# Performance work log

Measured on AMD Instinct MI355X. Metric: run time of the kernel, lower is better.

Reference implementation:

```python
import jax, jax.numpy as jnp
import numpy as np

N_NODES = 50000
N_EDGES = 800000
D_IN = 96
D_HID = 96
D_OUT = 4


def _glorot(key, shape):
    lim = float(np.sqrt(6.0 / (shape[0] + shape[1])))
    return jax.random.uniform(key, shape, jnp.float32, -lim, lim)


def setup_inputs() -> dict:
    key = jax.random.key(0)
    ks = jax.random.split(key, 8)
    x = jax.random.normal(ks[0], (N_NODES, D_IN), jnp.float32)
    edge_index = jax.random.randint(ks[1], (2, N_EDGES), 0, N_NODES, jnp.int64)
    return {
        'x': x,
        'edge_index': edge_index,
        'W0': _glorot(ks[2], (D_IN, D_HID)), 'b0': jnp.zeros((D_HID,), jnp.float32),
        'W1': _glorot(ks[3], (D_HID, D_HID)), 'b1': jnp.zeros((D_HID,), jnp.float32),
        'W2': _glorot(ks[4], (D_HID, D_HID)), 'b2': jnp.zeros((D_HID,), jnp.float32),
        'Wfc': _glorot(ks[5], (D_HID, D_OUT)), 'bfc': jnp.zeros((D_OUT,), jnp.float32),
    }


def _gcn_conv(x, src, dst, W, b, n):
    # GCNConv: linear transform, add self-loops, symmetric degree norm, scatter-add.
    h = x @ W                                   # [N, D]
    loops = jnp.arange(n, dtype=src.dtype)
    s = jnp.concatenate([src, loops])           # [E+N]
    d = jnp.concatenate([dst, loops])
    deg = jax.ops.segment_sum(jnp.ones_like(d, dtype=h.dtype), d, num_segments=n)
    dinv = jnp.where(deg > 0, jax.lax.rsqrt(deg), 0.0)
    norm = dinv[s] * dinv[d]                    # [E+N]
    msgs = h[s] * norm[:, None]                 # gather + scale
    out = jax.ops.segment_sum(msgs, d, num_segments=n)  # scatter-add
    return out + b


def reference(x, edge_index, W0, b0, W1, b1, W2, b2, Wfc, bfc):
    src, dst = edge_index[0], edge_index[1]
    n = x.shape[0]
    h = jax.nn.relu(_gcn_conv(x, src, dst, W0, b0, n))   # dropout = identity (eval)
    h = jax.nn.relu(_gcn_conv(h, src, dst, W1, b1, n))
    h = jax.nn.relu(_gcn_conv(h, src, dst, W2, b2, n))
    return h @ Wfc + bfc
```

## Files before the change

### kernel.cpp

```cpp
#include <hip/hip_runtime.h>

typedef __bf16 bf16x8 __attribute__((ext_vector_type(8)));
typedef float  f32x4  __attribute__((ext_vector_type(4)));
typedef float  f32x8  __attribute__((ext_vector_type(8)));
typedef unsigned short ushort;
typedef ushort us8 __attribute__((ext_vector_type(8)));

constexpr int N_NODES = 50000;
constexpr int N_EDGES = 800000;
constexpr int SLOTS = 64;
constexpr int GE   = N_EDGES / 256;
constexpr int WBLK = (3 * 9216) / 256;
constexpr int GMF  = (N_NODES + 63) / 64;

__device__ inline float h16f(ushort u) {
    union { _Float16 h; ushort u; } cv; cv.u = u; return (float)cv.h;
}
__device__ inline ushort f16b(float f) {
    union { _Float16 h; ushort u; } cv; cv.h = (_Float16)f; return cv.u;
}
__device__ inline ushort bf16b(float f) {
    union { __bf16 b; ushort u; } cv; cv.b = (__bf16)f; return cv.u;
}
__device__ inline f32x8 bf8_to_f32(us8 u) {
    f32x8 r;
#pragma unroll
    for (int i = 0; i < 8; ++i) r[i] = __uint_as_float(((unsigned int)u[i]) << 16);
    return r;
}

__global__ __launch_bounds__(256) void k_count(const int* __restrict__ dst,
                                               int* __restrict__ cnt,
                                               ushort* __restrict__ rank,
                                               const float* __restrict__ W0,
                                               const float* __restrict__ W1,
                                               const float* __restrict__ W2,
                                               ushort* __restrict__ Wt) {
    const int b = blockIdx.x;
    if (b < GE) {
        int e = b * 256 + threadIdx.x;
        rank[e] = (ushort)atomicAdd(&cnt[dst[e]], 1);
    } else {
        int i = (b - GE) * 256 + threadIdx.x;
        int m = i / 9216, li = i - m * 9216;
        const float* W = (m == 0) ? W0 : (m == 1) ? W1 : W2;
        int k = li / 96, c = li - k * 96;
        Wt[m * 9216 + c * 96 + k] = bf16b(W[li]);
    }
}

__device__ __forceinline__ void mfma_store(const ushort* sX, const ushort* sW,
                                           ushort* __restrict__ Y, int rowbase) {
    const int tid = threadIdx.x;
    const int wv = tid >> 6, lane = tid & 63, quad = lane >> 4, l16 = lane & 15;
    f32x4 acc[6];
#pragma unroll
    for (int t = 0; t < 6; ++t) acc[t] = (f32x4){0.f, 0.f, 0.f, 0.f};

    const ushort* ax = sX + (wv * 16 + l16) * 96 + quad * 8;
#pragma unroll
    for (int s = 0; s < 3; ++s) {
        bf16x8 a = *(const bf16x8*)(ax + s * 32);
#pragma unroll
        for (int t = 0; t < 6; ++t) {
            bf16x8 b = *(const bf16x8*)(sW + (t * 16 + l16) * 96 + s * 32 + quad * 8);
            acc[t] = __builtin_amdgcn_mfma_f32_16x16x32_bf16(a, b, acc[t], 0, 0, 0);
        }
    }
    const int r0 = rowbase + wv * 16 + quad * 4;
#pragma unroll
    for (int t = 0; t < 6; ++t) {
#pragma unroll
        for (int g = 0; g < 4; ++g) {
            int r = r0 + g;
            if (r < N_NODES) Y[(size_t)r * 96 + t * 16 + l16] = bf16b(acc[t][g]);
        }
    }
}

__global__ __launch_bounds__(256) void k_fill_gemm1(const int* __restrict__ src,
                                                    const int* __restrict__ dst,
                                                    const int* __restrict__ cnt,
                                                    const ushort* __restrict__ rank,
                                                    unsigned int* __restrict__ csr,
                                                    const float* __restrict__ x,
                                                    const ushort* __restrict__ Wt,
                                                    ushort* __restrict__ H) {
    __shared__ ushort sS[64 * 96 + 96 * 96];
    const int b = blockIdx.x;
    const int tid = threadIdx.x;
    if (b < GE) {
        int e = b * 256 + tid;
        int s = src[e], d = dst[e];
        float hs = rsqrtf((float)(cnt[s] + 1));
        unsigned int entry = (unsigned int)(ushort)s | ((unsigned int)f16b(hs) << 16);
        csr[(size_t)d * SLOTS + rank[e]] = entry;
    } else {
        ushort* sX = sS;
        ushort* sW = sS + 64 * 96;
        const int rowbase = (b - GE) * 64;
        for (int i = tid; i < 9216 / 8; i += 256)
            ((uint4*)sW)[i] = ((const uint4*)Wt)[i];
        for (int i = tid; i < 64 * 24; i += 256) {
            int r = i / 24, c4 = i % 24;
            int gr = rowbase + r;
            float4 v = make_float4(0.f, 0.f, 0.f, 0.f);
            if (gr < N_NODES) v = ((const float4*)(x + (size_t)gr * 96))[c4];
            ushort* p = sX + r * 96 + c4 * 4;
            p[0] = bf16b(v.x); p[1] = bf16b(v.y); p[2] = bf16b(v.z); p[3] = bf16b(v.w);
        }
        __syncthreads();
        mfma_store(sX, sW, H, rowbase);
    }
}

__global__ __launch_bounds__(768) void k_agg_gemm(const ushort* __restrict__ A,
                                                  const int* __restrict__ cnt,
                                                  const unsigned int* __restrict__ csr,
                                                  const float* __restrict__ bias,
                                                  const ushort* __restrict__ Wt,
                                                  ushort* __restrict__ Y) {
    __shared__ ushort sS[64 * 96 + 96 * 96];
    ushort* sX = sS;
    ushort* sW = sS + 64 * 96;
    const int tid = threadIdx.x;
    const int rowbase = blockIdx.x * 64;

    for (int i = tid; i < 9216 / 8; i += 768)
        ((uint4*)sW)[i] = ((const uint4*)Wt)[i];

    const int g = tid / 12;
    const int c = tid - g * 12;
    const int n = rowbase + g;

    f32x8 acc = (f32x8){0.f, 0.f, 0.f, 0.f, 0.f, 0.f, 0.f, 0.f};
    if (n < N_NODES) {
        const int deg = cnt[n];
        const float dn = rsqrtf((float)(deg + 1));
        us8 a0 = *(const us8*)(A + (size_t)n * 96 + c * 8);
        acc = bf8_to_f32(a0) * (dn * dn);

        const unsigned int* row = csr + (size_t)n * SLOTS;
        int j = 0;
        for (; j + 8 <= deg; j += 8) {
            const uint4 q0 = *(const uint4*)(row + j);
            const uint4 q1 = *(const uint4*)(row + j + 4);
            const us8 u0 = *(const us8*)(A + (size_t)(q0.x & 0xFFFFu) * 96 + c * 8);
            const us8 u1 = *(const us8*)(A + (size_t)(q0.y & 0xFFFFu) * 96 + c * 8);
            const us8 u2 = *(const us8*)(A + (size_t)(q0.z & 0xFFFFu) * 96 + c * 8);
            const us8 u3 = *(const us8*)(A + (size_t)(q0.w & 0xFFFFu) * 96 + c * 8);
            const us8 u4 = *(const us8*)(A + (size_t)(q1.x & 0xFFFFu) * 96 + c * 8);
            const us8 u5 = *(const us8*)(A + (size_t)(q1.y & 0xFFFFu) * 96 + c * 8);
            const us8 u6 = *(const us8*)(A + (size_t)(q1.z & 0xFFFFu) * 96 + c * 8);
            const us8 u7 = *(const us8*)(A + (size_t)(q1.w & 0xFFFFu) * 96 + c * 8);
            acc += bf8_to_f32(u0) * (h16f((ushort)(q0.x >> 16)) * dn);
            acc += bf8_to_f32(u1) * (h16f((ushort)(q0.y >> 16)) * dn);
            acc += bf8_to_f32(u2) * (h16f((ushort)(q0.z >> 16)) * dn);
            acc += bf8_to_f32(u3) * (h16f((ushort)(q0.w >> 16)) * dn);
            acc += bf8_to_f32(u4) * (h16f((ushort)(q1.x >> 16)) * dn);
            acc += bf8_to_f32(u5) * (h16f((ushort)(q1.y >> 16)) * dn);
            acc += bf8_to_f32(u6) * (h16f((ushort)(q1.z >> 16)) * dn);
            acc += bf8_to_f32(u7) * (h16f((ushort)(q1.w >> 16)) * dn);
        }
        for (; j + 4 <= deg; j += 4) {
            const uint4 q = *(const uint4*)(row + j);
            const us8 u0 = *(const us8*)(A + (size_t)(q.x & 0xFFFFu) * 96 + c * 8);
            const us8 u1 = *(const us8*)(A + (size_t)(q.y & 0xFFFFu) * 96 + c * 8);
            const us8 u2 = *(const us8*)(A + (size_t)(q.z & 0xFFFFu) * 96 + c * 8);
            const us8 u3 = *(const us8*)(A + (size_t)(q.w & 0xFFFFu) * 96 + c * 8);
            acc += bf8_to_f32(u0) * (h16f((ushort)(q.x >> 16)) * dn);
            acc += bf8_to_f32(u1) * (h16f((ushort)(q.y >> 16)) * dn);
            acc += bf8_to_f32(u2) * (h16f((ushort)(q.z >> 16)) * dn);
            acc += bf8_to_f32(u3) * (h16f((ushort)(q.w >> 16)) * dn);
        }
        for (; j < deg; ++j) {
            const unsigned int e = row[j];
            const float w = h16f((ushort)(e >> 16)) * dn;
            const us8 u = *(const us8*)(A + (size_t)(e & 0xFFFFu) * 96 + c * 8);
            acc += bf8_to_f32(u) * w;
        }
#pragma unroll
        for (int f = 0; f < 8; ++f) acc[f] = fmaxf(acc[f] + bias[c * 8 + f], 0.0f);
    }
    {
        us8 o;
#pragma unroll
        for (int f = 0; f < 8; ++f) o[f] = bf16b(acc[f]);
        *(us8*)(sX + g * 96 + c * 8) = o;
    }
    __syncthreads();

    const int wv = tid >> 6;
    const int lane = tid & 63, quad = lane >> 4, l16 = lane & 15;
    const int t0 = 2 * wv;
    const int rg = t0 / 6;
    const int ct0 = t0 - rg * 6;

    f32x4 acc0 = (f32x4){0.f, 0.f, 0.f, 0.f};
    f32x4 acc1 = (f32x4){0.f, 0.f, 0.f, 0.f};
    const ushort* ax = sX + (rg * 16 + l16) * 96 + quad * 8;
#pragma unroll
    for (int s = 0; s < 3; ++s) {
        bf16x8 a = *(const bf16x8*)(ax + s * 32);
        bf16x8 b0 = *(const bf16x8*)(sW + (ct0 * 16 + l16) * 96 + s * 32 + quad * 8);
        bf16x8 b1 = *(const bf16x8*)(sW + ((ct0 + 1) * 16 + l16) * 96 + s * 32 + quad * 8);
        acc0 = __builtin_amdgcn_mfma_f32_16x16x32_bf16(a, b0, acc0, 0, 0, 0);
        acc1 = __builtin_amdgcn_mfma_f32_16x16x32_bf16(a, b1, acc1, 0, 0, 0);
    }
    const int r0 = rowbase + rg * 16 + quad * 4;
#pragma unroll
    for (int gg = 0; gg < 4; ++gg) {
        int r = r0 + gg;
        if (r < N_NODES) {
            Y[(size_t)r * 96 + ct0 * 16 + l16]       = bf16b(acc0[gg]);
            Y[(size_t)r * 96 + (ct0 + 1) * 16 + l16] = bf16b(acc1[gg]);
        }
    }
}

template<int MODE>
__global__ __launch_bounds__(192) void k_agg(const ushort* __restrict__ A,
                                             const int* __restrict__ cnt,
                                             const unsigned int* __restrict__ csr,
                                             const float* __restrict__ bias,
                                             ushort* __restrict__ Hout,
                                             float* __restrict__ out4,
                                             const float* __restrict__ Wfc,
                                             const float* __restrict__ bfc) {
    __shared__ float sWfc[384];
    __shared__ float red[16][12][4];
    const int tid = threadIdx.x;
    if (MODE == 1) {
        for (int i = tid; i < 384; i += 192) sWfc[i] = Wfc[i];
        __syncthreads();
    }
    const int g = tid / 12, c = tid % 12;
    const int n = blockIdx.x * 16 + g;

    const int deg = cnt[n];
    const float dn = rsqrtf((float)(deg + 1));
    us8 a0 = *(const us8*)(A + (size_t)n * 96 + c * 8);
    f32x8 acc = bf8_to_f32(a0) * (dn * dn);

    const unsigned int* row = csr + (size_t)n * SLOTS;
    int j = 0;
    for (; j + 8 <= deg; j += 8) {
        const uint4 q0 = *(const uint4*)(row + j);
        const uint4 q1 = *(const uint4*)(row + j + 4);
        const us8 u0 = *(const us8*)(A + (size_t)(q0.x & 0xFFFFu) * 96 + c * 8);
        const us8 u1 = *(const us8*)(A + (size_t)(q0.y & 0xFFFFu) * 96 + c * 8);
        const us8 u2 = *(const us8*)(A + (size_t)(q0.z & 0xFFFFu) * 96 + c * 8);
        const us8 u3 = *(const us8*)(A + (size_t)(q0.w & 0xFFFFu) * 96 + c * 8);
        const us8 u4 = *(const us8*)(A + (size_t)(q1.x & 0xFFFFu) * 96 + c * 8);
        const us8 u5 = *(const us8*)(A + (size_t)(q1.y & 0xFFFFu) * 96 + c * 8);
        const us8 u6 = *(const us8*)(A + (size_t)(q1.z & 0xFFFFu) * 96 + c * 8);
        const us8 u7 = *(const us8*)(A + (size_t)(q1.w & 0xFFFFu) * 96 + c * 8);
        acc += bf8_to_f32(u0) * (h16f((ushort)(q0.x >> 16)) * dn);
        acc += bf8_to_f32(u1) * (h16f((ushort)(q0.y >> 16)) * dn);
        acc += bf8_to_f32(u2) * (h16f((ushort)(q0.z >> 16)) * dn);
        acc += bf8_to_f32(u3) * (h16f((ushort)(q0.w >> 16)) * dn);
        acc += bf8_to_f32(u4) * (h16f((ushort)(q1.x >> 16)) * dn);
        acc += bf8_to_f32(u5) * (h16f((ushort)(q1.y >> 16)) * dn);
        acc += bf8_to_f32(u6) * (h16f((ushort)(q1.z >> 16)) * dn);
        acc += bf8_to_f32(u7) * (h16f((ushort)(q1.w >> 16)) * dn);
    }
    for (; j + 4 <= deg; j += 4) {
        const uint4 q = *(const uint4*)(row + j);
        const us8 u0 = *(const us8*)(A + (size_t)(q.x & 0xFFFFu) * 96 + c * 8);
        const us8 u1 = *(const us8*)(A + (size_t)(q.y & 0xFFFFu) * 96 + c * 8);
        const us8 u2 = *(const us8*)(A + (size_t)(q.z & 0xFFFFu) * 96 + c * 8);
        const us8 u3 = *(const us8*)(A + (size_t)(q.w & 0xFFFFu) * 96 + c * 8);
        acc += bf8_to_f32(u0) * (h16f((ushort)(q.x >> 16)) * dn);
        acc += bf8_to_f32(u1) * (h16f((ushort)(q.y >> 16)) * dn);
        acc += bf8_to_f32(u2) * (h16f((ushort)(q.z >> 16)) * dn);
        acc += bf8_to_f32(u3) * (h16f((ushort)(q.w >> 16)) * dn);
    }
    for (; j < deg; ++j) {
        const unsigned int e = row[j];
        const float w = h16f((ushort)(e >> 16)) * dn;
        const us8 u = *(const us8*)(A + (size_t)(e & 0xFFFFu) * 96 + c * 8);
        acc += bf8_to_f32(u) * w;
    }
#pragma unroll
    for (int f = 0; f < 8; ++f) acc[f] = fmaxf(acc[f] + bias[c * 8 + f], 0.0f);

    if (MODE == 0) {
        us8 o;
#pragma unroll
        for (int f = 0; f < 8; ++f) o[f] = bf16b(acc[f]);
        *(us8*)(Hout + (size_t)n * 96 + c * 8) = o;
    } else {
        float p0 = 0.f, p1 = 0.f, p2 = 0.f, p3 = 0.f;
#pragma unroll
        for (int f = 0; f < 8; ++f) {
            const float* wr = sWfc + (c * 8 + f) * 4;
            p0 += acc[f] * wr[0];
            p1 += acc[f] * wr[1];
            p2 += acc[f] * wr[2];
            p3 += acc[f] * wr[3];
        }
        red[g][c][0] = p0; red[g][c][1] = p1; red[g][c][2] = p2; red[g][c][3] = p3;
        __syncthreads();
        if (tid < 64) {
            const int gg = tid >> 2, jj = tid & 3;
            float s = bfc[jj];
#pragma unroll
            for (int cc = 0; cc < 12; ++cc) s += red[gg][cc][jj];
            out4[(size_t)(blockIdx.x * 16 + gg) * 4 + jj] = s;
        }
    }
}

extern "C" void kernel_launch(void* const* d_in, const int* in_sizes, int n_in,
                              void* d_out, int out_size, void* d_ws, size_t ws_size,
                              hipStream_t stream) {
    const float* x   = (const float*)d_in[0];
    const int*   ei  = (const int*)d_in[1];
    const int*   src = ei;
    const int*   dst = ei + N_EDGES;
    const float* W0  = (const float*)d_in[2];
    const float* b0  = (const float*)d_in[3];
    const float* W1  = (const float*)d_in[4];
    const float* b1  = (const float*)d_in[5];
    const float* W2  = (const float*)d_in[6];
    const float* b2  = (const float*)d_in[7];
    const float* Wfc = (const float*)d_in[8];
    const float* bfc = (const float*)d_in[9];
    float* out = (float*)d_out;

    char* w = (char*)d_ws;
    unsigned int* csr = (unsigned int*)w;  w += ((size_t)N_NODES * SLOTS * 4 + 15) & ~15ULL;
    int*    cnt  = (int*)w;                w += ((size_t)N_NODES * 4 + 15) & ~15ULL;
    ushort* rank = (ushort*)w;             w += ((size_t)N_EDGES * 2 + 15) & ~15ULL;
    ushort* Wt   = (ushort*)w;             w += ((size_t)3 * 9216 * 2 + 15) & ~15ULL;
    ushort* H    = (ushort*)w;             w += ((size_t)N_NODES * 96 * 2 + 15) & ~15ULL;
    ushort* G    = (ushort*)w;

    const int gAgg = N_NODES / 16;

    (void)hipMemsetAsync(cnt, 0, (size_t)N_NODES * 4, stream);
    hipLaunchKernelGGL(k_count, dim3(GE + WBLK), dim3(256), 0, stream,
                       dst, cnt, rank, W0, W1, W2, Wt);
    hipLaunchKernelGGL(k_fill_gemm1, dim3(GE + GMF), dim3(256), 0, stream,
                       src, dst, cnt, rank, csr, x, Wt, H);
    hipLaunchKernelGGL(k_agg_gemm, dim3(GMF), dim3(768), 0, stream,
                       H, cnt, csr, b0, Wt + 9216, G);
    hipLaunchKernelGGL(k_agg_gemm, dim3(GMF), dim3(768), 0, stream,
                       G, cnt, csr, b1, Wt + 2 * 9216, H);
    hipLaunchKernelGGL((k_agg<1>), dim3(gAgg), dim3(192), 0, stream,
                       H, cnt, csr, b2, (ushort*)nullptr, out, Wfc, bfc);
}
```

Before: 224.5 us.

## Merge degree count and CSR fill into one pass, store 16-bit neighbor ids

Merges the count and fill kernels into one. Each edge atomically claims its slot and writes only a 16-bit source id, so the separate rank array and the precomputed fp16 per-edge norm go away. The aggregation kernels now look up the source degree from cnt for each neighbor instead of reading a packed norm, and they process 32 nodes per block with 384 threads. W0 is transposed inside each GEMM block, while W1 and W2 are converted by extra blocks. This drops one launch and halves CSR bytes, at the cost of an extra scattered cnt read per edge and redundant W0 conversion in every GEMM block.

```diff
diff --git a/kernel.cpp b/kernel.cpp
--- a/kernel.cpp
+++ b/kernel.cpp
@@ -5,20 +5,17 @@
 typedef float  f32x8  __attribute__((ext_vector_type(8)));
 typedef unsigned short ushort;
 typedef ushort us8 __attribute__((ext_vector_type(8)));
+typedef ushort us4 __attribute__((ext_vector_type(4)));
 
 constexpr int N_NODES = 50000;
 constexpr int N_EDGES = 800000;
 constexpr int SLOTS = 64;
 constexpr int GE   = N_EDGES / 256;
-constexpr int WBLK = (3 * 9216) / 256;
 constexpr int GMF  = (N_NODES + 63) / 64;
-
-__device__ inline float h16f(ushort u) {
-    union { _Float16 h; ushort u; } cv; cv.u = u; return (float)cv.h;
-}
-__device__ inline ushort f16b(float f) {
-    union { _Float16 h; ushort u; } cv; cv.h = (_Float16)f; return cv.u;
-}
+constexpr int WBLK = (2 * 9216) / 256;
+constexpr int AGG_NODES = 32;
+constexpr int GAGG = (N_NODES + AGG_NODES - 1) / AGG_NODES;
+
 __device__ inline ushort bf16b(float f) {
     union { __bf16 b; ushort u; } cv; cv.b = (__bf16)f; return cv.u;
 }
@@ -28,25 +25,8 @@
     for (int i = 0; i < 8; ++i) r[i] = __uint_as_float(((unsigned int)u[i]) << 16);
     return r;
 }
-
-__global__ __launch_bounds__(256) void k_count(const int* __restrict__ dst,
-                                               int* __restrict__ cnt,
-                                               ushort* __restrict__ rank,
-                                               const float* __restrict__ W0,
-                                               const float* __restrict__ W1,
-                                               const float* __restrict__ W2,
-                                               ushort* __restrict__ Wt) {
-    const int b = blockIdx.x;
-    if (b < GE) {
-        int e = b * 256 + threadIdx.x;
-        rank[e] = (ushort)atomicAdd(&cnt[dst[e]], 1);
-    } else {
-        int i = (b - GE) * 256 + threadIdx.x;
-        int m = i / 9216, li = i - m * 9216;
-        const float* W = (m == 0) ? W0 : (m == 1) ? W1 : W2;
-        int k = li / 96, c = li - k * 96;
-        Wt[m * 9216 + c * 96 + k] = bf16b(W[li]);
-    }
+__device__ inline float invdeg(const int* cnt, int s) {
+    return rsqrtf((float)(cnt[s] + 1));
 }
 
 __device__ __forceinline__ void mfma_store(const ushort* sX, const ushort* sW,
@@ -78,29 +58,32 @@
     }
 }
 
-__global__ __launch_bounds__(256) void k_fill_gemm1(const int* __restrict__ src,
-                                                    const int* __restrict__ dst,
-                                                    const int* __restrict__ cnt,
-                                                    const ushort* __restrict__ rank,
-                                                    unsigned int* __restrict__ csr,
-                                                    const float* __restrict__ x,
-                                                    const ushort* __restrict__ Wt,
-                                                    ushort* __restrict__ H) {
+__global__ __launch_bounds__(256) void k_count_gemm1(const int* __restrict__ src,
+                                                     const int* __restrict__ dst,
+                                                     int* __restrict__ cnt,
+                                                     ushort* __restrict__ csr,
+                                                     const float* __restrict__ x,
+                                                     const float* __restrict__ W0,
+                                                     const float* __restrict__ W1,
+                                                     const float* __restrict__ W2,
+                                                     ushort* __restrict__ Wt,
+                                                     ushort* __restrict__ H) {
     __shared__ ushort sS[64 * 96 + 96 * 96];
     const int b = blockIdx.x;
     const int tid = threadIdx.x;
     if (b < GE) {
         int e = b * 256 + tid;
-        int s = src[e], d = dst[e];
-        float hs = rsqrtf((float)(cnt[s] + 1));
-        unsigned int entry = (unsigned int)(ushort)s | ((unsigned int)f16b(hs) << 16);
-        csr[(size_t)d * SLOTS + rank[e]] = entry;
-    } else {
+        int d = dst[e];
+        int r = atomicAdd(&cnt[d], 1);
+        csr[(size_t)d * SLOTS + r] = (ushort)src[e];
+    } else if (b < GE + GMF) {
         ushort* sX = sS;
         ushort* sW = sS + 64 * 96;
         const int rowbase = (b - GE) * 64;
-        for (int i = tid; i < 9216 / 8; i += 256)
-            ((uint4*)sW)[i] = ((const uint4*)Wt)[i];
+        for (int i = tid; i < 9216; i += 256) {
+            int k = i / 96, cc = i - k * 96;
+            sW[cc * 96 + k] = bf16b(W0[i]);
+        }
         for (int i = tid; i < 64 * 24; i += 256) {
             int r = i / 24, c4 = i % 24;
             int gr = rowbase + r;
@@ -111,22 +94,28 @@
         }
         __syncthreads();
         mfma_store(sX, sW, H, rowbase);
-    }
-}
-
-__global__ __launch_bounds__(768) void k_agg_gemm(const ushort* __restrict__ A,
-                                                  const int* __restrict__ cnt,
-                                                  const unsigned int* __restrict__ csr,
-                                                  const float* __restrict__ bias,
-                                                  const ushort* __restrict__ Wt,
-                                                  ushort* __restrict__ Y) {
-    __shared__ ushort sS[64 * 96 + 96 * 96];
+    } else {
+        int i = (b - GE - GMF) * 256 + tid;
+        int m = i / 9216, li = i - m * 9216;
+        const float* W = (m == 0) ? W1 : W2;
+        int k = li / 96, cc = li - k * 96;
+        Wt[(m + 1) * 9216 + cc * 96 + k] = bf16b(W[li]);
+    }
+}
+
+__global__ __launch_bounds__(384, 4) void k_agg_gemm(const ushort* __restrict__ A,
+                                                     const int* __restrict__ cnt,
+                                                     const ushort* __restrict__ csr,
+                                                     const float* __restrict__ bias,
+                                                     const ushort* __restrict__ Wt,
+                                                     ushort* __restrict__ Y) {
+    __shared__ ushort sS[AGG_NODES * 96 + 96 * 96];
     ushort* sX = sS;
-    ushort* sW = sS + 64 * 96;
+    ushort* sW = sS + AGG_NODES * 96;
     const int tid = threadIdx.x;
-    const int rowbase = blockIdx.x * 64;
-
-    for (int i = tid; i < 9216 / 8; i += 768)
+    const int rowbase = blockIdx.x * AGG_NODES;
+
+    for (int i = tid; i < 9216 / 8; i += 384)
         ((uint4*)sW)[i] = ((const uint4*)Wt)[i];
 
     const int g = tid / 12;
@@ -138,47 +127,49 @@
         const int deg = cnt[n];
         const float dn = rsqrtf((float)(deg + 1));
         us8 a0 = *(const us8*)(A + (size_t)n * 96 + c * 8);
-        acc = bf8_to_f32(a0) * (dn * dn);
-
-        const unsigned int* row = csr + (size_t)n * SLOTS;
+
+        f32x8 nb = (f32x8){0.f, 0.f, 0.f, 0.f, 0.f, 0.f, 0.f, 0.f};
+        const ushort* row = csr + (size_t)n * SLOTS;
         int j = 0;
         for (; j + 8 <= deg; j += 8) {
-            const uint4 q0 = *(const uint4*)(row + j);
-            const uint4 q1 = *(const uint4*)(row + j + 4);
-            const us8 u0 = *(const us8*)(A + (size_t)(q0.x & 0xFFFFu) * 96 + c * 8);
-            const us8 u1 = *(const us8*)(A + (size_t)(q0.y & 0xFFFFu) * 96 + c * 8);
-            const us8 u2 = *(const us8*)(A + (size_t)(q0.z & 0xFFFFu) * 96 + c * 8);
-            const us8 u3 = *(const us8*)(A + (size_t)(q0.w & 0xFFFFu) * 96 + c * 8);
-            const us8 u4 = *(const us8*)(A + (size_t)(q1.x & 0xFFFFu) * 96 + c * 8);
-            const us8 u5 = *(const us8*)(A + (size_t)(q1.y & 0xFFFFu) * 96 + c * 8);
-            const us8 u6 = *(const us8*)(A + (size_t)(q1.z & 0xFFFFu) * 96 + c * 8);
-            const us8 u7 = *(const us8*)(A + (size_t)(q1.w & 0xFFFFu) * 96 + c * 8);
-            acc += bf8_to_f32(u0) * (h16f((ushort)(q0.x >> 16)) * dn);
-            acc += bf8_to_f32(u1) * (h16f((ushort)(q0.y >> 16)) * dn);
-            acc += bf8_to_f32(u2) * (h16f((ushort)(q0.z >> 16)) * dn);
-            acc += bf8_to_f32(u3) * (h16f((ushort)(q0.w >> 16)) * dn);
-            acc += bf8_to_f32(u4) * (h16f((ushort)(q1.x >> 16)) * dn);
-            acc += bf8_to_f32(u5) * (h16f((ushort)(q1.y >> 16)) * dn);
-            acc += bf8_to_f32(u6) * (h16f((ushort)(q1.z >> 16)) * dn);
-            acc += bf8_to_f32(u7) * (h16f((ushort)(q1.w >> 16)) * dn);
+            const us8 q = *(const us8*)(row + j);
+            const int s0 = q[0], s1 = q[1], s2 = q[2], s3 = q[3];
+            const int s4 = q[4], s5 = q[5], s6 = q[6], s7 = q[7];
+            const us8 u0 = *(const us8*)(A + (size_t)s0 * 96 + c * 8);
+            const us8 u1 = *(const us8*)(A + (size_t)s1 * 96 + c * 8);
+            const us8 u2 = *(const us8*)(A + (size_t)s2 * 96 + c * 8);
+            const us8 u3 = *(const us8*)(A + (size_t)s3 * 96 + c * 8);
+            const us8 u4 = *(const us8*)(A + (size_t)s4 * 96 + c * 8);
+            const us8 u5 = *(const us8*)(A + (size_t)s5 * 96 + c * 8);
+            const us8 u6 = *(const us8*)(A + (size_t)s6 * 96 + c * 8);
+            const us8 u7 = *(const us8*)(A + (size_t)s7 * 96 + c * 8);
+            nb += bf8_to_f32(u0) * invdeg(cnt, s0);
+            nb += bf8_to_f32(u1) * invdeg(cnt, s1);
+            nb += bf8_to_f32(u2) * invdeg(cnt, s2);
+            nb += bf8_to_f32(u3) * invdeg(cnt, s3);
+            nb += bf8_to_f32(u4) * invdeg(cnt, s4);
+            nb += bf8_to_f32(u5) * invdeg(cnt, s5);
+            nb += bf8_to_f32(u6) * invdeg(cnt, s6);
+            nb += bf8_to_f32(u7) * invdeg(cnt, s7);
         }
         for (; j + 4 <= deg; j += 4) {
-            const uint4 q = *(const uint4*)(row + j);
-            const us8 u0 = *(const us8*)(A + (size_t)(q.x & 0xFFFFu) * 96 + c * 8);
-            const us8 u1 = *(const us8*)(A + (size_t)(q.y & 0xFFFFu) * 96 + c * 8);
-            const us8 u2 = *(const us8*)(A + (size_t)(q.z & 0xFFFFu) * 96 + c * 8);
-            const us8 u3 = *(const us8*)(A + (size_t)(q.w & 0xFFFFu) * 96 + c * 8);
-            acc += bf8_to_f32(u0) * (h16f((ushort)(q.x >> 16)) * dn);
-            acc += bf8_to_f32(u1) * (h16f((ushort)(q.y >> 16)) * dn);
-            acc += bf8_to_f32(u2) * (h16f((ushort)(q.z >> 16)) * dn);
-            acc += bf8_to_f32(u3) * (h16f((ushort)(q.w >> 16)) * dn);
+            const us4 q = *(const us4*)(row + j);
+            const int s0 = q[0], s1 = q[1], s2 = q[2], s3 = q[3];
+            const us8 u0 = *(const us8*)(A + (size_t)s0 * 96 + c * 8);
+            const us8 u1 = *(const us8*)(A + (size_t)s1 * 96 + c * 8);
+            const us8 u2 = *(const us8*)(A + (size_t)s2 * 96 + c * 8);
+            const us8 u3 = *(const us8*)(A + (size_t)s3 * 96 + c * 8);
+            nb += bf8_to_f32(u0) * invdeg(cnt, s0);
+            nb += bf8_to_f32(u1) * invdeg(cnt, s1);
+            nb += bf8_to_f32(u2) * invdeg(cnt, s2);
+            nb += bf8_to_f32(u3) * invdeg(cnt, s3);
         }
         for (; j < deg; ++j) {
-            const unsigned int e = row[j];
-            const float w = h16f((ushort)(e >> 16)) * dn;
-            const us8 u = *(const us8*)(A + (size_t)(e & 0xFFFFu) * 96 + c * 8);
-            acc += bf8_to_f32(u) * w;
-        }
+            const int s = row[j];
+            const us8 u = *(const us8*)(A + (size_t)s * 96 + c * 8);
+            nb += bf8_to_f32(u) * invdeg(cnt, s);
+        }
+        acc = (nb + bf8_to_f32(a0) * dn) * dn;
 #pragma unroll
         for (int f = 0; f < 8; ++f) acc[f] = fmaxf(acc[f] + bias[c * 8 + f], 0.0f);
     }
@@ -218,96 +209,87 @@
     }
 }
 
-template<int MODE>
-__global__ __launch_bounds__(192) void k_agg(const ushort* __restrict__ A,
-                                             const int* __restrict__ cnt,
-                                             const unsigned int* __restrict__ csr,
-                                             const float* __restrict__ bias,
-                                             ushort* __restrict__ Hout,
-                                             float* __restrict__ out4,
-                                             const float* __restrict__ Wfc,
-                                             const float* __restrict__ bfc) {
+__global__ __launch_bounds__(192) void k_agg_fc(const ushort* __restrict__ A,
+                                                const int* __restrict__ cnt,
+                                                const ushort* __restrict__ csr,
+                                                const float* __restrict__ bias,
+                                                float* __restrict__ out4,
+                                                const float* __restrict__ Wfc,
+                                                const float* __restrict__ bfc) {
     __shared__ float sWfc[384];
     __shared__ float red[16][12][4];
     const int tid = threadIdx.x;
-    if (MODE == 1) {
-        for (int i = tid; i < 384; i += 192) sWfc[i] = Wfc[i];
-        __syncthreads();
-    }
+    for (int i = tid; i < 384; i += 192) sWfc[i] = Wfc[i];
+    __syncthreads();
     const int g = tid / 12, c = tid % 12;
     const int n = blockIdx.x * 16 + g;
 
     const int deg = cnt[n];
     const float dn = rsqrtf((float)(deg + 1));
     us8 a0 = *(const us8*)(A + (size_t)n * 96 + c * 8);
-    f32x8 acc = bf8_to_f32(a0) * (dn * dn);
-
-    const unsigned int* row = csr + (size_t)n * SLOTS;
+
+    f32x8 nb = (f32x8){0.f, 0.f, 0.f, 0.f, 0.f, 0.f, 0.f, 0.f};
+    const ushort* row = csr + (size_t)n * SLOTS;
     int j = 0;
     for (; j + 8 <= deg; j += 8) {
-        const uint4 q0 = *(const uint4*)(row + j);
-        const uint4 q1 = *(const uint4*)(row + j + 4);
-        const us8 u0 = *(const us8*)(A + (size_t)(q0.x & 0xFFFFu) * 96 + c * 8);
-        const us8 u1 = *(const us8*)(A + (size_t)(q0.y & 0xFFFFu) * 96 + c * 8);
-        const us8 u2 = *(const us8*)(A + (size_t)(q0.z & 0xFFFFu) * 96 + c * 8);
-        const us8 u3 = *(const us8*)(A + (size_t)(q0.w & 0xFFFFu) * 96 + c * 8);
-        const us8 u4 = *(const us8*)(A + (size_t)(q1.x & 0xFFFFu) * 96 + c * 8);
-        const us8 u5 = *(const us8*)(A + (size_t)(q1.y & 0xFFFFu) * 96 + c * 8);
-        const us8 u6 = *(const us8*)(A + (size_t)(q1.z & 0xFFFFu) * 96 + c * 8);
-        const us8 u7 = *(const us8*)(A + (size_t)(q1.w & 0xFFFFu) * 96 + c * 8);
-        acc += bf8_to_f32(u0) * (h16f((ushort)(q0.x >> 16)) * dn);
-        acc += bf8_to_f32(u1) * (h16f((ushort)(q0.y >> 16)) * dn);
-        acc += bf8_to_f32(u2) * (h16f((ushort)(q0.z >> 16)) * dn);
-        acc += bf8_to_f32(u3) * (h16f((ushort)(q0.w >> 16)) * dn);
-        acc += bf8_to_f32(u4) * (h16f((ushort)(q1.x >> 16)) * dn);
-        acc += bf8_to_f32(u5) * (h16f((ushort)(q1.y >> 16)) * dn);
-        acc += bf8_to_f32(u6) * (h16f((ushort)(q1.z >> 16)) * dn);
-        acc += bf8_to_f32(u7) * (h16f((ushort)(q1.w >> 16)) * dn);
+        const us8 q = *(const us8*)(row + j);
+        const int s0 = q[0], s1 = q[1], s2 = q[2], s3 = q[3];
+        const int s4 = q[4], s5 = q[5], s6 = q[6], s7 = q[7];
+        const us8 u0 = *(const us8*)(A + (size_t)s0 * 96 + c * 8);
+        const us8 u1 = *(const us8*)(A + (size_t)s1 * 96 + c * 8);
+        const us8 u2 = *(const us8*)(A + (size_t)s2 * 96 + c * 8);
+        const us8 u3 = *(const us8*)(A + (size_t)s3 * 96 + c * 8);
+        const us8 u4 = *(const us8*)(A + (size_t)s4 * 96 + c * 8);
+        const us8 u5 = *(const us8*)(A + (size_t)s5 * 96 + c * 8);
+        const us8 u6 = *(const us8*)(A + (size_t)s6 * 96 + c * 8);
+        const us8 u7 = *(const us8*)(A + (size_t)s7 * 96 + c * 8);
+        nb += bf8_to_f32(u0) * invdeg(cnt, s0);
+        nb += bf8_to_f32(u1) * invdeg(cnt, s1);
+        nb += bf8_to_f32(u2) * invdeg(cnt, s2);
+        nb += bf8_to_f32(u3) * invdeg(cnt, s3);
+        nb += bf8_to_f32(u4) * invdeg(cnt, s4);
+        nb += bf8_to_f32(u5) * invdeg(cnt, s5);
+        nb += bf8_to_f32(u6) * invdeg(cnt, s6);
+        nb += bf8_to_f32(u7) * invdeg(cnt, s7);
     }
     for (; j + 4 <= deg; j += 4) {
-        const uint4 q = *(const uint4*)(row + j);
-        const us8 u0 = *(const us8*)(A + (size_t)(q.x & 0xFFFFu) * 96 + c * 8);
-        const us8 u1 = *(const us8*)(A + (size_t)(q.y & 0xFFFFu) * 96 + c * 8);
-        const us8 u2 = *(const us8*)(A + (size_t)(q.z & 0xFFFFu) * 96 + c * 8);
-        const us8 u3 = *(const us8*)(A + (size_t)(q.w & 0xFFFFu) * 96 + c * 8);
-        acc += bf8_to_f32(u0) * (h16f((ushort)(q.x >> 16)) * dn);
-        acc += bf8_to_f32(u1) * (h16f((ushort)(q.y >> 16)) * dn);
-        acc += bf8_to_f32(u2) * (h16f((ushort)(q.z >> 16)) * dn);
-        acc += bf8_to_f32(u3) * (h16f((ushort)(q.w >> 16)) * dn);
+        const us4 q = *(const us4*)(row + j);
+        const int s0 = q[0], s1 = q[1], s2 = q[2], s3 = q[3];
+        const us8 u0 = *(const us8*)(A + (size_t)s0 * 96 + c * 8);
+        const us8 u1 = *(const us8*)(A + (size_t)s1 * 96 + c * 8);
+        const us8 u2 = *(const us8*)(A + (size_t)s2 * 96 + c * 8);
+        const us8 u3 = *(const us8*)(A + (size_t)s3 * 96 + c * 8);
+        nb += bf8_to_f32(u0) * invdeg(cnt, s0);
+        nb += bf8_to_f32(u1) * invdeg(cnt, s1);
+        nb += bf8_to_f32(u2) * invdeg(cnt, s2);
+        nb += bf8_to_f32(u3) * invdeg(cnt, s3);
     }
     for (; j < deg; ++j) {
-        const unsigned int e = row[j];
-        const float w = h16f((ushort)(e >> 16)) * dn;
-        const us8 u = *(const us8*)(A + (size_t)(e & 0xFFFFu) * 96 + c * 8);
-        acc += bf8_to_f32(u) * w;
-    }
+        const int s = row[j];
+        const us8 u = *(const us8*)(A + (size_t)s * 96 + c * 8);
+        nb += bf8_to_f32(u) * invdeg(cnt, s);
+    }
+    f32x8 acc = (nb + bf8_to_f32(a0) * dn) * dn;
 #pragma unroll
     for (int f = 0; f < 8; ++f) acc[f] = fmaxf(acc[f] + bias[c * 8 + f], 0.0f);
 
-    if (MODE == 0) {
-        us8 o;
-#pragma unroll
-        for (int f = 0; f < 8; ++f) o[f] = bf16b(acc[f]);
-        *(us8*)(Hout + (size_t)n * 96 + c * 8) = o;
-    } else {
-        float p0 = 0.f, p1 = 0.f, p2 = 0.f, p3 = 0.f;
-#pragma unroll
-        for (int f = 0; f < 8; ++f) {
-            const float* wr = sWfc + (c * 8 + f) * 4;
-            p0 += acc[f] * wr[0];
-            p1 += acc[f] * wr[1];
-            p2 += acc[f] * wr[2];
-            p3 += acc[f] * wr[3];
-        }
-        red[g][c][0] = p0; red[g][c][1] = p1; red[g][c][2] = p2; red[g][c][3] = p3;
-        __syncthreads();
-        if (tid < 64) {
-            const int gg = tid >> 2, jj = tid & 3;
-            float s = bfc[jj];
-#pragma unroll
-            for (int cc = 0; cc < 12; ++cc) s += red[gg][cc][jj];
-            out4[(size_t)(blockIdx.x * 16 + gg) * 4 + jj] = s;
-        }
+    float p0 = 0.f, p1 = 0.f, p2 = 0.f, p3 = 0.f;
+#pragma unroll
+    for (int f = 0; f < 8; ++f) {
+        const float* wr = sWfc + (c * 8 + f) * 4;
+        p0 += acc[f] * wr[0];
+        p1 += acc[f] * wr[1];
+        p2 += acc[f] * wr[2];
+        p3 += acc[f] * wr[3];
+    }
+    red[g][c][0] = p0; red[g][c][1] = p1; red[g][c][2] = p2; red[g][c][3] = p3;
+    __syncthreads();
+    if (tid < 64) {
+        const int gg = tid >> 2, jj = tid & 3;
+        float s = bfc[jj];
+#pragma unroll
+        for (int cc = 0; cc < 12; ++cc) s += red[gg][cc][jj];
+        out4[(size_t)(blockIdx.x * 16 + gg) * 4 + jj] = s;
     }
 }
 
@@ -329,24 +311,19 @@
     float* out = (float*)d_out;
 
     char* w = (char*)d_ws;
-    unsigned int* csr = (unsigned int*)w;  w += ((size_t)N_NODES * SLOTS * 4 + 15) & ~15ULL;
+    ushort* csr = (ushort*)w;              w += ((size_t)N_NODES * SLOTS * 2 + 15) & ~15ULL;
     int*    cnt  = (int*)w;                w += ((size_t)N_NODES * 4 + 15) & ~15ULL;
-    ushort* rank = (ushort*)w;             w += ((size_t)N_EDGES * 2 + 15) & ~15ULL;
     ushort* Wt   = (ushort*)w;             w += ((size_t)3 * 9216 * 2 + 15) & ~15ULL;
     ushort* H    = (ushort*)w;             w += ((size_t)N_NODES * 96 * 2 + 15) & ~15ULL;
     ushort* G    = (ushort*)w;
 
-    const int gAgg = N_NODES / 16;
-
     (void)hipMemsetAsync(cnt, 0, (size_t)N_NODES * 4, stream);
-    hipLaunchKernelGGL(k_count, dim3(GE + WBLK), dim3(256), 0, stream,
-                       dst, cnt, rank, W0, W1, W2, Wt);
-    hipLaunchKernelGGL(k_fill_gemm1, dim3(GE + GMF), dim3(256), 0, stream,
-                       src, dst, cnt, rank, csr, x, Wt, H);
-    hipLaunchKernelGGL(k_agg_gemm, dim3(GMF), dim3(768), 0, stream,
+    hipLaunchKernelGGL(k_count_gemm1, dim3(GE + GMF + WBLK), dim3(256), 0, stream,
+                       src, dst, cnt, csr, x, W0, W1, W2, Wt, H);
+    hipLaunchKernelGGL(k_agg_gemm, dim3(GAGG), dim3(384), 0, stream,
                        H, cnt, csr, b0, Wt + 9216, G);
-    hipLaunchKernelGGL(k_agg_gemm, dim3(GMF), dim3(768), 0, stream,
+    hipLaunchKernelGGL(k_agg_gemm, dim3(GAGG), dim3(384), 0, stream,
                        G, cnt, csr, b1, Wt + 2 * 9216, H);
-    hipLaunchKernelGGL((k_agg<1>), dim3(gAgg), dim3(192), 0, stream,
-                       H, cnt, csr, b2, (ushort*)nullptr, out, Wfc, bfc);
-}
+    hipLaunchKernelGGL(k_agg_fc, dim3(N_NODES / 16), dim3(192), 0, stream,
+                       H, cnt, csr, b2, out, Wfc, bfc);
+}
```

New measurement: 253.9 us. +13.1%, slower.
